# Performance work log

Hardware: AMD Instinct MI355X
Metric: run time of the kernel (lower is better)

## Reference

```python
import jax, jax.numpy as jnp
import numpy as np

IN_C, HID_C, OUT_C = 128, 256, 128
N_NODES, N_EDGES = 50000, 600000


def setup_inputs() -> dict:
    key = jax.random.key(0)
    ks = jax.random.split(key, 8)
    x = jax.random.normal(ks[0], (N_NODES, IN_C), dtype=jnp.float32)
    edge_index = jax.random.randint(ks[1], (2, N_EDGES), 0, N_NODES, dtype=jnp.int64)
    def glorot(k, shape):
        lim = np.sqrt(6.0 / (shape[0] + shape[1])).astype(np.float32)
        return jax.random.uniform(k, shape, dtype=jnp.float32, minval=-lim, maxval=lim)
    # PyG SAGEConv: out = lin_l(mean_aggr) + lin_r(x_root); bias only in lin_l
    W1_l = glorot(ks[2], (IN_C, HID_C)); b1 = jnp.zeros((HID_C,), jnp.float32)
    W1_r = glorot(ks[3], (IN_C, HID_C))
    W2_l = glorot(ks[4], (HID_C, OUT_C)); b2 = jnp.zeros((OUT_C,), jnp.float32)
    W2_r = glorot(ks[5], (HID_C, OUT_C))
    return {"x": x, "edge_index": edge_index, "W1_l": W1_l, "b1": b1, "W1_r": W1_r,
            "W2_l": W2_l, "b2": b2, "W2_r": W2_r}


def _sage_conv(x, src, dst, W_l, b, W_r):
    n = x.shape[0]
    msg = x[src]  # [E, C] gather from source nodes
    agg = jax.ops.segment_sum(msg, dst, num_segments=n)
    cnt = jax.ops.segment_sum(jnp.ones((src.shape[0],), x.dtype), dst, num_segments=n)
    agg = agg / jnp.maximum(cnt, 1.0)[:, None]  # mean aggregation, zero-deg safe
    return agg @ W_l + b + x @ W_r


def reference(x, edge_index, W1_l, b1, W1_r, W2_l, b2, W2_r):
    src, dst = edge_index[0], edge_index[1]
    h = jax.nn.relu(_sage_conv(x, src, dst, W1_l, b1, W1_r))
    return _sage_conv(h, src, dst, W2_l, b2, W2_r)
```

## Files before the change

kernel.cpp:

```cpp
#include <hip/hip_runtime.h>
#include <hip/hip_bf16.h>


#define N_NODES 50000
#define IN_C    128
#define HID_C   256
#define OUT_C   128
#define N_EDGES 600000

#define PB_CNT  2344
#define PB_W1   (PB_CNT + 256)
#define PB_W2   (PB_W1 + 256)
#define PB_X    (PB_W2 + 6250)

typedef __attribute__((ext_vector_type(8))) short short8;
typedef __attribute__((ext_vector_type(4))) float f32x4;
typedef __attribute__((ext_vector_type(2))) float f32x2;

__device__ __forceinline__ float bf2f(short s) {
    union { unsigned u; float f; } c;
    c.u = ((unsigned)(unsigned short)s) << 16;
    return c.f;
}
__device__ __forceinline__ unsigned f2fp8(float v) {
    return (unsigned)__builtin_amdgcn_cvt_pk_fp8_f32(v, v, 0, false) & 0xffu;
}
__device__ __forceinline__ void acc_fp8x4(float* a, unsigned u) {
    f32x2 lo = __builtin_amdgcn_cvt_pk_f32_fp8(u, false);
    f32x2 hi = __builtin_amdgcn_cvt_pk_f32_fp8(u, true);
    a[0] += lo[0]; a[1] += lo[1]; a[2] += hi[0]; a[3] += hi[1];
}

__global__ __launch_bounds__(256) void prep(
    const float* __restrict__ x, __hip_bfloat16* __restrict__ A1,
    const float* __restrict__ W1l, const float* __restrict__ W1r,
    const float* __restrict__ W2l, const float* __restrict__ W2r,
    __hip_bfloat16* __restrict__ W1t, __hip_bfloat16* __restrict__ W2t,
    const int* __restrict__ dstI, int* __restrict__ cnt) {
    int b = blockIdx.x;
    if (b < PB_CNT) {
        int e = b * 256 + threadIdx.x;
        if (e < N_EDGES) atomicAdd(&cnt[dstI[e]], 1);
    } else if (b < PB_W1) {
        int reg = b - PB_CNT;
        int half = reg >> 7;
        int t = (reg & 127) * 256 + threadIdx.x;
        int k = t >> 8, n = t & 255;
        const float* src = half ? W1r : W1l;
        W1t[n * 256 + half * 128 + k] = __float2bfloat16(src[t]);
    } else if (b < PB_W2) {
        int reg = b - PB_W1;
        int half = reg >> 7;
        int t = (reg & 127) * 256 + threadIdx.x;
        int k = t >> 7, n = t & 127;
        const float* src = half ? W2r : W2l;
        W2t[(size_t)(half * 128 + n) * 256 + k] = __float2bfloat16(src[t]);
    } else {
        int t = (b - PB_W2) * 256 + threadIdx.x;
        if (t >= N_NODES * 32) return;
        int row = t >> 5, c = (t & 31) * 4;
        float4 v = *(const float4*)(x + (size_t)row * 128 + c);
        __hip_bfloat16* d = A1 + (size_t)row * 256 + 128 + c;
        __hip_bfloat162 p0, p1;
        p0.x = __float2bfloat16(v.x); p0.y = __float2bfloat16(v.y);
        p1.x = __float2bfloat16(v.z); p1.y = __float2bfloat16(v.w);
        *(__hip_bfloat162*)d = p0;
        *(__hip_bfloat162*)(d + 2) = p1;
    }
}

__global__ __launch_bounds__(256) void assign_offsets(
    const int* __restrict__ cnt, int* __restrict__ row_ptr,
    int* __restrict__ cursor, int* __restrict__ total, int n) {
    __shared__ int tmp[256];
    __shared__ int sbase;
    int t = threadIdx.x, g = blockIdx.x * 256 + t;
    int v = (g < n) ? cnt[g] : 0;
    tmp[t] = v; __syncthreads();
    for (int off = 1; off < 256; off <<= 1) {
        int u = (t >= off) ? tmp[t - off] : 0;
        __syncthreads();
        tmp[t] += u;
        __syncthreads();
    }
    if (t == 255) sbase = atomicAdd(total, tmp[255]);
    __syncthreads();
    if (g < n) {
        int e = sbase + tmp[t] - v;
        row_ptr[g] = e;
        cursor[g] = e;
    }
}

__global__ void fill_csr(const int* __restrict__ srcI, const int* __restrict__ dstI,
                         int* __restrict__ cursor, int* __restrict__ col, int E) {
    int e = blockIdx.x * blockDim.x + threadIdx.x;
    if (e < E) {
        int pos = atomicAdd(&cursor[dstI[e]], 1);
        col[pos] = srcI[e];
    }
}

__global__ __launch_bounds__(256) void aggregate_bf16(
    const __hip_bfloat16* __restrict__ feat, int featStride,
    const int* __restrict__ row_ptr, const int* __restrict__ deg,
    const int* __restrict__ col,
    __hip_bfloat16* __restrict__ outp, int outStride, int nNodes) {
    int node = blockIdx.x * 16 + (threadIdx.x >> 4);
    int sl   = threadIdx.x & 15;
    if (node >= nNodes) return;
    int beg = row_ptr[node];
    int d   = deg[node];
    const __hip_bfloat16* base = feat + sl * 8;
    float a[8];
    #pragma unroll
    for (int c = 0; c < 8; ++c) a[c] = 0.f;

    short8 v0, v1, v2, v3;
    int j = 0;
    if (d >= 4) {
        int s0 = col[beg + 0], s1 = col[beg + 1];
        int s2 = col[beg + 2], s3 = col[beg + 3];
        v0 = *(const short8*)(base + (size_t)s0 * featStride);
        v1 = *(const short8*)(base + (size_t)s1 * featStride);
        v2 = *(const short8*)(base + (size_t)s2 * featStride);
        v3 = *(const short8*)(base + (size_t)s3 * featStride);
        for (; j + 8 <= d; j += 4) {
            int t0 = col[beg + j + 4], t1 = col[beg + j + 5];
            int t2 = col[beg + j + 6], t3 = col[beg + j + 7];
            short8 w0 = *(const short8*)(base + (size_t)t0 * featStride);
            short8 w1 = *(const short8*)(base + (size_t)t1 * featStride);
            short8 w2 = *(const short8*)(base + (size_t)t2 * featStride);
            short8 w3 = *(const short8*)(base + (size_t)t3 * featStride);
            #pragma unroll
            for (int c = 0; c < 8; ++c)
                a[c] += (bf2f(v0[c]) + bf2f(v1[c])) + (bf2f(v2[c]) + bf2f(v3[c]));
            v0 = w0; v1 = w1; v2 = w2; v3 = w3;
        }
        #pragma unroll
        for (int c = 0; c < 8; ++c)
            a[c] += (bf2f(v0[c]) + bf2f(v1[c])) + (bf2f(v2[c]) + bf2f(v3[c]));
        j += 4;
    }
    int rem = d - j;
    if (rem > 0) {
        int s0 = col[beg + j];
        int s1 = (rem > 1) ? col[beg + j + 1] : s0;
        int s2 = (rem > 2) ? col[beg + j + 2] : s0;
        short8 t0 = *(const short8*)(base + (size_t)s0 * featStride);
        short8 t1 = *(const short8*)(base + (size_t)s1 * featStride);
        short8 t2 = *(const short8*)(base + (size_t)s2 * featStride);
        #pragma unroll
        for (int c = 0; c < 8; ++c) a[c] += bf2f(t0[c]);
        if (rem > 1) {
            #pragma unroll
            for (int c = 0; c < 8; ++c) a[c] += bf2f(t1[c]);
        }
        if (rem > 2) {
            #pragma unroll
            for (int c = 0; c < 8; ++c) a[c] += bf2f(t2[c]);
        }
    }

    float inv = 1.f / (float)max(d, 1);
    __hip_bfloat16* o = outp + (size_t)node * outStride + sl * 8;
    short8 q;
    #pragma unroll
    for (int c = 0; c < 8; ++c) {
        union { __hip_bfloat16 b; short s; } cv;
        cv.b = __float2bfloat16(a[c] * inv);
        q[c] = cv.s;
    }
    *(short8*)o = q;
}

__global__ __launch_bounds__(256) void aggregate_fp8_final(
    const unsigned char* __restrict__ feat,
    const int* __restrict__ row_ptr, const int* __restrict__ deg,
    const int* __restrict__ col,
    float* __restrict__ outp, const float* __restrict__ pre, int nNodes) {
    int node = blockIdx.x * 16 + (threadIdx.x >> 4);
    int sl   = threadIdx.x & 15;
    if (node >= nNodes) return;
    int beg = row_ptr[node];
    int d   = deg[node];
    const unsigned char* base = feat + sl * 8;
    float a[8];
    #pragma unroll
    for (int c = 0; c < 8; ++c) a[c] = 0.f;

    uint2 v0, v1, v2, v3;
    int j = 0;
    if (d >= 4) {
        int s0 = col[beg + 0], s1 = col[beg + 1];
        int s2 = col[beg + 2], s3 = col[beg + 3];
        v0 = *(const uint2*)(base + (size_t)s0 * 128);
        v1 = *(const uint2*)(base + (size_t)s1 * 128);
        v2 = *(const uint2*)(base + (size_t)s2 * 128);
        v3 = *(const uint2*)(base + (size_t)s3 * 128);
        for (; j + 8 <= d; j += 4) {
            int t0 = col[beg + j + 4], t1 = col[beg + j + 5];
            int t2 = col[beg + j + 6], t3 = col[beg + j + 7];
            uint2 w0 = *(const uint2*)(base + (size_t)t0 * 128);
            uint2 w1 = *(const uint2*)(base + (size_t)t1 * 128);
            uint2 w2 = *(const uint2*)(base + (size_t)t2 * 128);
            uint2 w3 = *(const uint2*)(base + (size_t)t3 * 128);
            acc_fp8x4(a,     v0.x); acc_fp8x4(a,     v1.x);
            acc_fp8x4(a,     v2.x); acc_fp8x4(a,     v3.x);
            acc_fp8x4(a + 4, v0.y); acc_fp8x4(a + 4, v1.y);
            acc_fp8x4(a + 4, v2.y); acc_fp8x4(a + 4, v3.y);
            v0 = w0; v1 = w1; v2 = w2; v3 = w3;
        }
        acc_fp8x4(a,     v0.x); acc_fp8x4(a,     v1.x);
        acc_fp8x4(a,     v2.x); acc_fp8x4(a,     v3.x);
        acc_fp8x4(a + 4, v0.y); acc_fp8x4(a + 4, v1.y);
        acc_fp8x4(a + 4, v2.y); acc_fp8x4(a + 4, v3.y);
        j += 4;
    }
    for (; j < d; ++j) {
        uint2 v = *(const uint2*)(base + (size_t)col[beg + j] * 128);
        acc_fp8x4(a, v.x);
        acc_fp8x4(a + 4, v.y);
    }

    float inv = 1.f / (float)max(d, 1);
    const float* pp = pre + (size_t)node * 128 + sl * 8;
    float* op = outp + (size_t)node * 128 + sl * 8;
    float4 p0 = *(const float4*)pp;
    float4 p1 = *(const float4*)(pp + 4);
    *(float4*)op       = make_float4(a[0] * inv + p0.x, a[1] * inv + p0.y,
                                     a[2] * inv + p0.z, a[3] * inv + p0.w);
    *(float4*)(op + 4) = make_float4(a[4] * inv + p1.x, a[5] * inv + p1.y,
                                     a[6] * inv + p1.z, a[7] * inv + p1.w);
}


#define GBM 128
#define GBN 128
#define GBK 64
#define EP_STRIDE_BF 132
#define EP_STRIDE_F8 136

__device__ __forceinline__ void gload16(const void* g, void* l) {
    typedef const __attribute__((address_space(1))) unsigned int* gp_t;
    typedef __attribute__((address_space(3))) unsigned int* lp_t;
    __builtin_amdgcn_global_load_lds((gp_t)g, (lp_t)l, 16, 0, 0);
}

__global__ __launch_bounds__(256) void gemm_mfma(
    const __hip_bfloat16* __restrict__ A, int lda,
    const __hip_bfloat16* __restrict__ Bt,
    const float* __restrict__ bias,
    __hip_bfloat16* __restrict__ outBf,
    unsigned char* __restrict__ outF8,
    float* __restrict__ outF,
    int M, int K, int mode) {
    __shared__ char sm[GBM * EP_STRIDE_BF * 2];
    __hip_bfloat16* Als = (__hip_bfloat16*)sm;
    __hip_bfloat16* Bls = (__hip_bfloat16*)(sm + GBM * GBK * 2);

    int tid  = threadIdx.x;
    int wave = tid >> 6, lane = tid & 63;
    int wm = wave >> 1, wn = wave & 1;
    int mb = blockIdx.x * GBM, nb = blockIdx.y * GBN;

    int srow_base = wave * 32;
    int lrow = lane >> 3;
    int pch  = lane & 7;

    f32x4 acc[4][4];
    #pragma unroll
    for (int i = 0; i < 4; ++i)
        #pragma unroll
        for (int j = 0; j < 4; ++j)
            acc[i][j] = (f32x4){0.f, 0.f, 0.f, 0.f};

    for (int kt = 0; kt < K; kt += GBK) {
        #pragma unroll
        for (int t = 0; t < 4; ++t) {
            int rloc = srow_base + t * 8 + lrow;
            int lch  = pch ^ (rloc & 7);
            int ga_row = mb + rloc; if (ga_row >= M) ga_row = M - 1;
            const __hip_bfloat16* ga = A + (size_t)ga_row * lda + kt + lch * 8;
            gload16(ga, &Als[(srow_base + t * 8) * GBK]);
            const __hip_bfloat16* gb = Bt + (size_t)(nb + rloc) * K + kt + lch * 8;
            gload16(gb, &Bls[(srow_base + t * 8) * GBK]);
        }
        __syncthreads();

        #pragma unroll
        for (int ks = 0; ks < GBK; ks += 32) {
            int chunkL = (ks >> 3) + (lane >> 4);
            short8 af[4], bf[4];
            #pragma unroll
            for (int i = 0; i < 4; ++i) {
                int row = wm * 64 + i * 16 + (lane & 15);
                int pc  = chunkL ^ (row & 7);
                af[i] = *(const short8*)&Als[row * GBK + pc * 8];
            }
            #pragma unroll
            for (int j = 0; j < 4; ++j) {
                int row = wn * 64 + j * 16 + (lane & 15);
                int pc  = chunkL ^ (row & 7);
                bf[j] = *(const short8*)&Bls[row * GBK + pc * 8];
            }
            #pragma unroll
            for (int i = 0; i < 4; ++i)
                #pragma unroll
                for (int j = 0; j < 4; ++j)
                    acc[i][j] = __builtin_amdgcn_mfma_f32_16x16x32_bf16(
                        af[i], bf[j], acc[i][j], 0, 0, 0);
        }
        __syncthreads();
    }

    int cn[4];
    float bc[4];
    #pragma unroll
    for (int j = 0; j < 4; ++j) {
        cn[j] = wn * 64 + j * 16 + (lane & 15);
        bc[j] = 0.f;
    }
    if (mode == 0) {
        __hip_bfloat16* sb = (__hip_bfloat16*)sm;
        #pragma unroll
        for (int j = 0; j < 4; ++j) bc[j] = bias[nb + cn[j]];
        #pragma unroll
        for (int i = 0; i < 4; ++i)
            #pragma unroll
            for (int r = 0; r < 4; ++r) {
                int lr = wm * 64 + i * 16 + (lane >> 4) * 4 + r;
                #pragma unroll
                for (int j = 0; j < 4; ++j)
                    sb[lr * EP_STRIDE_BF + cn[j]] =
                        __float2bfloat16(fmaxf(acc[i][j][r] + bc[j], 0.f));
            }
        __syncthreads();
        #pragma unroll
        for (int it = 0; it < 8; ++it) {
            int chunk = it * 256 + tid;
            int lr  = chunk >> 4;
            int lcB = (chunk & 15) * 16;
            int grow = mb + lr;
            if (grow < M)
                *(float4*)((char*)outBf + (size_t)grow * 512 + nb * 2 + lcB) =
                    *(const float4*)((const char*)sb + lr * (EP_STRIDE_BF * 2) + lcB);
        }
    } else if (blockIdx.y == 0) {
        unsigned char* s8 = (unsigned char*)sm;
        #pragma unroll
        for (int i = 0; i < 4; ++i)
            #pragma unroll
            for (int r = 0; r < 4; ++r) {
                int lr = wm * 64 + i * 16 + (lane >> 4) * 4 + r;
                #pragma unroll
                for (int j = 0; j < 4; ++j)
                    s8[lr * EP_STRIDE_F8 + cn[j]] = (unsigned char)f2fp8(acc[i][j][r]);
            }
        __syncthreads();
        #pragma unroll
        for (int it = 0; it < 4; ++it) {
            int chunk = it * 256 + tid;
            int lr  = chunk >> 3;
            int lcB = (chunk & 7) * 16;
            int grow = mb + lr;
            if (grow < M)
                *(float4*)(outF8 + (size_t)grow * 128 + lcB) =
                    *(const float4*)(s8 + lr * EP_STRIDE_F8 + lcB);
        }
    } else {
        #pragma unroll
        for (int j = 0; j < 4; ++j) bc[j] = bias[cn[j]];
        #pragma unroll
        for (int i = 0; i < 4; ++i)
            #pragma unroll
            for (int r = 0; r < 4; ++r) {
                int row = mb + wm * 64 + i * 16 + (lane >> 4) * 4 + r;
                if (row >= M) continue;
                #pragma unroll
                for (int j = 0; j < 4; ++j)
                    outF[(size_t)row * 128 + cn[j]] = acc[i][j][r] + bc[j];
            }
    }
}

extern "C" void kernel_launch(void* const* d_in, const int* in_sizes, int n_in,
                              void* d_out, int out_size, void* d_ws, size_t ws_size,
                              hipStream_t stream) {
    const float* x    = (const float*)d_in[0];
    const int*   ei   = (const int*)d_in[1];
    const float* W1l  = (const float*)d_in[2];
    const float* b1   = (const float*)d_in[3];
    const float* W1r  = (const float*)d_in[4];
    const float* W2l  = (const float*)d_in[5];
    const float* b2   = (const float*)d_in[6];
    const float* W2r  = (const float*)d_in[7];
    float* out = (float*)d_out;

    const int E = N_EDGES;
    const int N = N_NODES;
    const int* srcI = ei;
    const int* dstI = ei + E;

    char* w = (char*)d_ws;
    int*            cnt     = (int*)(w + 0);
    int*            total   = (int*)(w + 200000);
    int*            row_ptr = (int*)(w + 204800);
    int*            col     = (int*)(w + 409600);
    __hip_bfloat16* W1t     = (__hip_bfloat16*)(w + 2818048);
    __hip_bfloat16* W2t     = (__hip_bfloat16*)(w + 2949120);
    int*            cursor  = (int*)(w + 3080192);
    __hip_bfloat16* A1      = (__hip_bfloat16*)(w + 3280896);
    __hip_bfloat16* h_bf    = (__hip_bfloat16*)(w + 28880896);
    unsigned char*  hp_f8   = (unsigned char*)(w + 54480896);
    float*          pre     = (float*)(w + 67280896);

    hipMemsetAsync(cnt, 0, 200004, stream);
    prep<<<PB_X, 256, 0, stream>>>(x, A1, W1l, W1r, W2l, W2r, W1t, W2t, dstI, cnt);

    assign_offsets<<<(N + 255) / 256, 256, 0, stream>>>(cnt, row_ptr, cursor, total, N);
    fill_csr<<<(E + 255) / 256, 256, 0, stream>>>(srcI, dstI, cursor, col, E);

    aggregate_bf16<<<(N + 15) / 16, 256, 0, stream>>>(
        A1 + 128, 256, row_ptr, cnt, col, A1, 256, N);
    {
        dim3 grid((N + GBM - 1) / GBM, HID_C / GBN);
        gemm_mfma<<<grid, 256, 0, stream>>>(A1, 256, W1t, b1,
                                            h_bf, nullptr, nullptr, N, 256, 0);
    }

    {
        dim3 grid((N + GBM - 1) / GBM, 2);
        gemm_mfma<<<grid, 256, 0, stream>>>(h_bf, 256, W2t, b2,
                                            nullptr, hp_f8, pre, N, 256, 1);
    }
    aggregate_fp8_final<<<(N + 15) / 16, 256, 0, stream>>>(
        hp_f8, row_ptr, cnt, col, out, pre, N);
}
```

Baseline: 234.8 us.

## Replace second GEMM with 64x256 tile kernel producing fp8 and fp32 halves

```diff
diff --git a/kernel.cpp b/kernel.cpp
--- a/kernel.cpp
+++ b/kernel.cpp
@@ -239,7 +239,6 @@
 #define GBN 128
 #define GBK 64
 #define EP_STRIDE_BF 132
-#define EP_STRIDE_F8 136
 
 __device__ __forceinline__ void gload16(const void* g, void* l) {
     typedef const __attribute__((address_space(1))) unsigned int* gp_t;
@@ -252,9 +251,7 @@
     const __hip_bfloat16* __restrict__ Bt,
     const float* __restrict__ bias,
     __hip_bfloat16* __restrict__ outBf,
-    unsigned char* __restrict__ outF8,
-    float* __restrict__ outF,
-    int M, int K, int mode) {
+    int M, int K) {
     __shared__ char sm[GBM * EP_STRIDE_BF * 2];
     __hip_bfloat16* Als = (__hip_bfloat16*)sm;
     __hip_bfloat16* Bls = (__hip_bfloat16*)(sm + GBM * GBK * 2);
@@ -316,70 +313,131 @@
 
     int cn[4];
     float bc[4];
+    __hip_bfloat16* sb = (__hip_bfloat16*)sm;
     #pragma unroll
     for (int j = 0; j < 4; ++j) {
         cn[j] = wn * 64 + j * 16 + (lane & 15);
-        bc[j] = 0.f;
-    }
-    if (mode == 0) {
-        __hip_bfloat16* sb = (__hip_bfloat16*)sm;
-        #pragma unroll
-        for (int j = 0; j < 4; ++j) bc[j] = bias[nb + cn[j]];
-        #pragma unroll
-        for (int i = 0; i < 4; ++i)
-            #pragma unroll
-            for (int r = 0; r < 4; ++r) {
-                int lr = wm * 64 + i * 16 + (lane >> 4) * 4 + r;
+        bc[j] = bias[nb + cn[j]];
+    }
+    #pragma unroll
+    for (int i = 0; i < 4; ++i)
+        #pragma unroll
+        for (int r = 0; r < 4; ++r) {
+            int lr = wm * 64 + i * 16 + (lane >> 4) * 4 + r;
+            #pragma unroll
+            for (int j = 0; j < 4; ++j)
+                sb[lr * EP_STRIDE_BF + cn[j]] =
+                    __float2bfloat16(fmaxf(acc[i][j][r] + bc[j], 0.f));
+        }
+    __syncthreads();
+    #pragma unroll
+    for (int it = 0; it < 8; ++it) {
+        int chunk = it * 256 + tid;
+        int lr  = chunk >> 4;
+        int lcB = (chunk & 15) * 16;
+        int grow = mb + lr;
+        if (grow < M)
+            *(float4*)((char*)outBf + (size_t)grow * 512 + nb * 2 + lcB) =
+                *(const float4*)((const char*)sb + lr * (EP_STRIDE_BF * 2) + lcB);
+    }
+}
+
+#define GBM2 64
+
+__global__ __launch_bounds__(256) void gemm2_fused(
+    const __hip_bfloat16* __restrict__ A,
+    const __hip_bfloat16* __restrict__ Bt,
+    const float* __restrict__ b2,
+    unsigned char* __restrict__ outF8,
+    float* __restrict__ outF,
+    int M) {
+    __shared__ __hip_bfloat16 Als[GBM2 * GBK];
+    __shared__ __hip_bfloat16 Bls[256 * GBK];
+
+    int tid  = threadIdx.x;
+    int wave = tid >> 6, lane = tid & 63;
+    int mb = blockIdx.x * GBM2;
+    int lrow = lane >> 3;
+    int pch  = lane & 7;
+
+    f32x4 acc[4][4];
+    #pragma unroll
+    for (int i = 0; i < 4; ++i)
+        #pragma unroll
+        for (int j = 0; j < 4; ++j)
+            acc[i][j] = (f32x4){0.f, 0.f, 0.f, 0.f};
+
+    for (int kt = 0; kt < 256; kt += GBK) {
+        #pragma unroll
+        for (int t = 0; t < 2; ++t) {
+            int g = wave * 2 + t;
+            int rloc = g * 8 + lrow;
+            int lch  = pch ^ (rloc & 7);
+            int ga_row = mb + rloc; if (ga_row >= M) ga_row = M - 1;
+            gload16(A + (size_t)ga_row * 256 + kt + lch * 8, &Als[g * 8 * GBK]);
+        }
+        #pragma unroll
+        for (int t = 0; t < 8; ++t) {
+            int g = wave * 8 + t;
+            int rloc = g * 8 + lrow;
+            int lch  = pch ^ (rloc & 7);
+            gload16(Bt + (size_t)rloc * 256 + kt + lch * 8, &Bls[g * 8 * GBK]);
+        }
+        __syncthreads();
+
+        #pragma unroll
+        for (int ks = 0; ks < GBK; ks += 32) {
+            int chunkL = (ks >> 3) + (lane >> 4);
+            short8 af[4], bf[4];
+            #pragma unroll
+            for (int i = 0; i < 4; ++i) {
+                int row = i * 16 + (lane & 15);
+                int pc  = chunkL ^ (row & 7);
+                af[i] = *(const short8*)&Als[row * GBK + pc * 8];
+            }
+            #pragma unroll
+            for (int j = 0; j < 4; ++j) {
+                int row = wave * 64 + j * 16 + (lane & 15);
+                int pc  = chunkL ^ (row & 7);
+                bf[j] = *(const short8*)&Bls[row * GBK + pc * 8];
+            }
+            #pragma unroll
+            for (int i = 0; i < 4; ++i)
                 #pragma unroll
                 for (int j = 0; j < 4; ++j)
-                    sb[lr * EP_STRIDE_BF + cn[j]] =
-                        __float2bfloat16(fmaxf(acc[i][j][r] + bc[j], 0.f));
-            }
-        __syncthreads();
-        #pragma unroll
-        for (int it = 0; it < 8; ++it) {
-            int chunk = it * 256 + tid;
-            int lr  = chunk >> 4;
-            int lcB = (chunk & 15) * 16;
-            int grow = mb + lr;
-            if (grow < M)
-                *(float4*)((char*)outBf + (size_t)grow * 512 + nb * 2 + lcB) =
-                    *(const float4*)((const char*)sb + lr * (EP_STRIDE_BF * 2) + lcB);
-        }
-    } else if (blockIdx.y == 0) {
-        unsigned char* s8 = (unsigned char*)sm;
+                    acc[i][j] = __builtin_amdgcn_mfma_f32_16x16x32_bf16(
+                        af[i], bf[j], acc[i][j], 0, 0, 0);
+        }
+        __syncthreads();
+    }
+
+    int cn[4];
+    #pragma unroll
+    for (int j = 0; j < 4; ++j) cn[j] = wave * 64 + j * 16 + (lane & 15);
+    if (wave < 2) {
         #pragma unroll
         for (int i = 0; i < 4; ++i)
             #pragma unroll
             for (int r = 0; r < 4; ++r) {
-                int lr = wm * 64 + i * 16 + (lane >> 4) * 4 + r;
-                #pragma unroll
-                for (int j = 0; j < 4; ++j)
-                    s8[lr * EP_STRIDE_F8 + cn[j]] = (unsigned char)f2fp8(acc[i][j][r]);
-            }
-        __syncthreads();
-        #pragma unroll
-        for (int it = 0; it < 4; ++it) {
-            int chunk = it * 256 + tid;
-            int lr  = chunk >> 3;
-            int lcB = (chunk & 7) * 16;
-            int grow = mb + lr;
-            if (grow < M)
-                *(float4*)(outF8 + (size_t)grow * 128 + lcB) =
-                    *(const float4*)(s8 + lr * EP_STRIDE_F8 + lcB);
-        }
-    } else {
-        #pragma unroll
-        for (int j = 0; j < 4; ++j) bc[j] = bias[cn[j]];
-        #pragma unroll
-        for (int i = 0; i < 4; ++i)
-            #pragma unroll
-            for (int r = 0; r < 4; ++r) {
-                int row = mb + wm * 64 + i * 16 + (lane >> 4) * 4 + r;
+                int row = mb + i * 16 + (lane >> 4) * 4 + r;
                 if (row >= M) continue;
                 #pragma unroll
                 for (int j = 0; j < 4; ++j)
-                    outF[(size_t)row * 128 + cn[j]] = acc[i][j][r] + bc[j];
+                    outF8[(size_t)row * 128 + cn[j]] = (unsigned char)f2fp8(acc[i][j][r]);
+            }
+    } else {
+        float bc[4];
+        #pragma unroll
+        for (int j = 0; j < 4; ++j) bc[j] = b2[cn[j] - 128];
+        #pragma unroll
+        for (int i = 0; i < 4; ++i)
+            #pragma unroll
+            for (int r = 0; r < 4; ++r) {
+                int row = mb + i * 16 + (lane >> 4) * 4 + r;
+                if (row >= M) continue;
+                #pragma unroll
+                for (int j = 0; j < 4; ++j)
+                    outF[(size_t)row * 128 + cn[j] - 128] = acc[i][j][r] + bc[j];
             }
     }
 }
@@ -425,15 +483,12 @@
         A1 + 128, 256, row_ptr, cnt, col, A1, 256, N);
     {
         dim3 grid((N + GBM - 1) / GBM, HID_C / GBN);
-        gemm_mfma<<<grid, 256, 0, stream>>>(A1, 256, W1t, b1,
-                                            h_bf, nullptr, nullptr, N, 256, 0);
-    }
-
-    {
-        dim3 grid((N + GBM - 1) / GBM, 2);
-        gemm_mfma<<<grid, 256, 0, stream>>>(h_bf, 256, W2t, b2,
-                                            nullptr, hp_f8, pre, N, 256, 1);
-    }
+        gemm_mfma<<<grid, 256, 0, stream>>>(A1, 256, W1t, b1, h_bf, N, 256);
+    }
+
+    gemm2_fused<<<(N + GBM2 - 1) / GBM2, 256, 0, stream>>>(
+        h_bf, W2t, b2, hp_f8, pre, N);
+
     aggregate_fp8_final<<<(N + 15) / 16, 256, 0, stream>>>(
         hp_f8, row_ptr, cnt, col, out, pre, N);
 }
```

After: 232.2 us. Within noise of the previous version (-1.1%).
